# Optimization experiments

Hardware: AMD Instinct MI355X
Metric: run time of the kernel (lower is better)

The kernel has to match this reference:

```python
import jax, jax.numpy as jnp
import numpy as np

# Standard SMPL kinematic tree (parent of each of the 24 joints)
PARENTS = np.array([-1, 0, 0, 0, 1, 2, 3, 4, 5, 6, 7, 8, 9, 9, 9, 12, 13, 14, 16, 17, 18, 19, 20, 21])
B, V, NJ = 512, 6890, 24


def rodrigues(r):
    # r: (N,3) axis-angle -> (N,3,3) rotation matrices
    theta = jnp.linalg.norm(r, axis=1, keepdims=True) + 1e-8  # (N,1), eps mirrors the noise trick in torch code
    rh = r / theta                                            # (N,3) unit axis
    x, y, z = rh[:, 0], rh[:, 1], rh[:, 2]
    zero = jnp.zeros_like(x)
    K = jnp.stack([zero, -z, y, z, zero, -x, -y, x, zero], axis=1).reshape(-1, 3, 3)
    cos = jnp.cos(theta)[:, :, None]
    sin = jnp.sin(theta)[:, :, None]
    outer = rh[:, :, None] * rh[:, None, :]
    I3 = jnp.eye(3, dtype=r.dtype)
    return cos * I3 + (1.0 - cos) * outer + sin * K


def _make_A(Ri, ti):
    # Ri: (B,3,3), ti: (B,3) -> homogeneous (B,4,4)
    Rt = jnp.concatenate([Ri, ti[:, :, None]], axis=2)  # (B,3,4)
    bottom = jnp.broadcast_to(jnp.array([0.0, 0.0, 0.0, 1.0], dtype=Ri.dtype), (Ri.shape[0], 1, 4))
    return jnp.concatenate([Rt, bottom], axis=1)


def smpl_forward(betas, pose, trans, v_template, shapedirs, posedirs, J_regressor, joint_regressor, weights):
    b = betas.shape[0]
    # shape blend shapes
    v_shaped = jnp.einsum('bs,vcs->bvc', betas, shapedirs) + v_template  # (B,V,3)
    J = jnp.einsum('jv,bvc->bjc', J_regressor, v_shaped)                 # (B,24,3)
    R = rodrigues(pose.reshape(-1, 3)).reshape(b, NJ, 3, 3)              # (B,24,3,3)
    I3 = jnp.eye(3, dtype=pose.dtype)
    lrotmin = (R[:, 1:] - I3).reshape(b, (NJ - 1) * 9)                   # (B,207)
    v_posed = v_shaped + jnp.einsum('bp,vcp->bvc', lrotmin, posedirs)    # pose blend shapes
    # forward kinematics along the chain (fixed 24-joint loop)
    Gs = [_make_A(R[:, 0], J[:, 0])]
    for i in range(1, NJ):
        p = int(PARENTS[i])
        Gs.append(jnp.matmul(Gs[p], _make_A(R[:, i], J[:, i] - J[:, p])))
    G = jnp.stack(Gs, axis=1)                                            # (B,24,4,4)
    # remove rest-pose joint locations (the 'pack' subtraction)
    Jh = jnp.concatenate([J, jnp.zeros((b, NJ, 1), dtype=J.dtype)], axis=2)  # (B,24,4)
    t = jnp.einsum('bjxy,bjy->bjx', G, Jh)                               # (B,24,4)
    G = G - jnp.pad(t[..., None], ((0, 0), (0, 0), (0, 0), (3, 0)))      # subtract in last column
    # linear blend skinning
    T = jnp.einsum('bjxy,vj->bvxy', G, weights)                          # (B,V,4,4) -- large, memory bound
    vh = jnp.concatenate([v_posed, jnp.ones((b, v_posed.shape[1], 1), dtype=v_posed.dtype)], axis=2)
    v = jnp.einsum('bvxy,bvy->bvx', T, vh)[..., :3]                      # (B,V,3)
    result = v + trans[:, None, :]
    joints = jnp.einsum('bvc,jv->bjc', result, joint_regressor)          # (B,24,3)
    return result, joints


def setup_inputs() -> dict:
    key = jax.random.key(0)
    ks = jax.random.split(key, 9)
    betas = jax.random.normal(ks[0], (B, 10), dtype=jnp.float32)
    pose = jax.random.normal(ks[1], (B, 72), dtype=jnp.float32) * 0.3
    trans = jax.random.normal(ks[2], (B, 3), dtype=jnp.float32)
    v_template = jax.random.normal(ks[3], (V, 3), dtype=jnp.float32) * 0.3
    shapedirs = jax.random.normal(ks[4], (V, 3, 10), dtype=jnp.float32) * 0.01
    posedirs = jax.random.normal(ks[5], (V, 3, 207), dtype=jnp.float32) * 0.01
    Jr = jax.random.uniform(ks[6], (NJ, V), dtype=jnp.float32)
    J_regressor = Jr / jnp.sum(Jr, axis=1, keepdims=True)
    jr2 = jax.random.uniform(ks[7], (NJ, V), dtype=jnp.float32)
    joint_regressor = jr2 / jnp.sum(jr2, axis=1, keepdims=True)
    w = jax.random.uniform(ks[8], (V, NJ), dtype=jnp.float32)
    weights = w / jnp.sum(w, axis=1, keepdims=True)
    return {"betas": betas, "pose": pose, "trans": trans, "v_template": v_template,
            "shapedirs": shapedirs, "posedirs": posedirs, "J_regressor": J_regressor,
            "joint_regressor": joint_regressor, "weights": weights}


def reference(betas, pose, trans, v_template, shapedirs, posedirs, J_regressor, joint_regressor, weights):
    return smpl_forward(betas, pose, trans, v_template, shapedirs, posedirs, J_regressor, joint_regressor, weights)
```

## Files before the change

kernel.cpp:

```cpp
#include <hip/hip_runtime.h>
#include <hip/hip_bf16.h>

#define VNUM 6890
#define VPAD 6912
#define BNUM 512
#define NJ 24

typedef short bf16x8 __attribute__((ext_vector_type(8)));
typedef float f32x4 __attribute__((ext_vector_type(4)));

__device__ __forceinline__ short f2bf(float x) {
    union { float f; unsigned u; } v; v.f = x;
    unsigned r = v.u + 0x7fff + ((v.u >> 16) & 1);
    return (short)(r >> 16);
}

#define WS_JS 0
#define WS_LWX 800
#define WS_GA 58144
#define WS_WT 156448
#define WS_PB 267040
#define WS_PART 267040

#define RES_ELEMS (512 * 6890 * 3)

__global__ __launch_bounds__(256) void ka_kernel(const float* __restrict__ Jr,
                                                 const float* __restrict__ sd,
                                                 const float* __restrict__ vt,
                                                 float* __restrict__ part) {
    int j = blockIdx.x;
    int ch = blockIdx.y;
    int tid = threadIdx.x;
    int vbeg = ch * 864;
    int vend = min(vbeg + 864, VNUM);
    float acc[33];
#pragma unroll
    for (int k = 0; k < 33; ++k) acc[k] = 0.f;
    for (int v = vbeg + tid; v < vend; v += 256) {
        float q = Jr[j * VNUM + v];
#pragma unroll
        for (int c = 0; c < 3; ++c) {
#pragma unroll
            for (int s = 0; s < 10; ++s)
                acc[c * 11 + s] += q * sd[v * 30 + c * 10 + s];
            acc[c * 11 + 10] += q * vt[v * 3 + c];
        }
    }
#pragma unroll
    for (int k = 0; k < 33; ++k) {
        float a = acc[k];
#pragma unroll
        for (int off = 32; off >= 1; off >>= 1) a += __shfl_xor(a, off);
        acc[k] = a;
    }
    __shared__ float red[4][33];
    int lane = tid & 63, wid = tid >> 6;
    if (lane == 0) {
#pragma unroll
        for (int k = 0; k < 33; ++k) red[wid][k] = acc[k];
    }
    __syncthreads();
    if (tid < 33)
        part[(j * 8 + ch) * 33 + tid] = red[0][tid] + red[1][tid] + red[2][tid] + red[3][tid];
}

__global__ __launch_bounds__(64) void ka2_kernel(const float* __restrict__ part,
                                                 float* __restrict__ js) {
    int j = blockIdx.x;
    int t = threadIdx.x;
    if (t < 33) {
        float a = 0.f;
#pragma unroll
        for (int ch = 0; ch < 8; ++ch) a += part[(j * 8 + ch) * 33 + t];
        js[j * 33 + t] = a;
    }
}

__global__ __launch_bounds__(64) void kb_kernel(const float* __restrict__ pose,
                                                const float* __restrict__ betas,
                                                const float* __restrict__ trans,
                                                const float* __restrict__ js,
                                                short* __restrict__ lwX,
                                                short* __restrict__ ga) {
    int b = blockIdx.x;
    int t = threadIdx.x;
    __shared__ float Rl[24][9];
    __shared__ float Jl[24][3];
    __shared__ float Gl[24][12];

    if (t < 24) {
        float x = pose[b * 72 + t * 3 + 0];
        float y = pose[b * 72 + t * 3 + 1];
        float z = pose[b * 72 + t * 3 + 2];
        float th = sqrtf(x * x + y * y + z * z) + 1e-8f;
        float rx = x / th, ry = y / th, rz = z / th;
        float cs = cosf(th), sn = sinf(th), mc = 1.f - cs;
        float R[9];
        R[0] = cs + mc * rx * rx;      R[1] = mc * rx * ry - sn * rz; R[2] = mc * rx * rz + sn * ry;
        R[3] = mc * ry * rx + sn * rz; R[4] = cs + mc * ry * ry;      R[5] = mc * ry * rz - sn * rx;
        R[6] = mc * rz * rx - sn * ry; R[7] = mc * rz * ry + sn * rx; R[8] = cs + mc * rz * rz;
#pragma unroll
        for (int k = 0; k < 9; ++k) Rl[t][k] = R[k];
        if (t >= 1) {
#pragma unroll
            for (int k = 0; k < 9; ++k)
                lwX[b * 224 + (t - 1) * 9 + k] =
                    f2bf(R[k] - ((k == 0 || k == 4 || k == 8) ? 1.f : 0.f));
        }
#pragma unroll
        for (int c = 0; c < 3; ++c) {
            float a = js[(t * 3 + c) * 11 + 10];
#pragma unroll
            for (int s = 0; s < 10; ++s) a += betas[b * 10 + s] * js[(t * 3 + c) * 11 + s];
            Jl[t][c] = a;
        }
    } else if (t >= 32 && t < 42) {
        lwX[b * 224 + 207 + (t - 32)] = f2bf(betas[b * 10 + (t - 32)]);
    } else if (t == 42) {
        lwX[b * 224 + 217] = f2bf(1.f);
    } else if (t >= 43 && t < 49) {
        lwX[b * 224 + 218 + (t - 43)] = 0;
    }
    __syncthreads();

    if (t < 12) {
        int x = t >> 2, yy = t & 3;
        Gl[0][t] = (yy < 3) ? Rl[0][x * 3 + yy] : Jl[0][x];
    }
    __syncthreads();

    const int par[24] = {-1, 0, 0, 0, 1, 2, 3, 4, 5, 6, 7, 8, 9, 9, 9, 12, 13, 14, 16, 17, 18, 19, 20, 21};
#pragma unroll
    for (int i = 1; i < 24; ++i) {
        if (t < 12) {
            int x = t >> 2, yy = t & 3;
            int p = par[i];
            float a0, a1, a2, add;
            if (yy < 3) {
                a0 = Rl[i][0 * 3 + yy]; a1 = Rl[i][1 * 3 + yy]; a2 = Rl[i][2 * 3 + yy]; add = 0.f;
            } else {
                a0 = Jl[i][0] - Jl[p][0]; a1 = Jl[i][1] - Jl[p][1]; a2 = Jl[i][2] - Jl[p][2];
                add = Gl[p][x * 4 + 3];
            }
            Gl[i][t] = Gl[p][x * 4 + 0] * a0 + Gl[p][x * 4 + 1] * a1 + Gl[p][x * 4 + 2] * a2 + add;
        }
        __syncthreads();
    }

    if (t < 24) {
#pragma unroll
        for (int x = 0; x < 3; ++x) {
            float tx = Gl[t][x * 4 + 0] * Jl[t][0] + Gl[t][x * 4 + 1] * Jl[t][1] + Gl[t][x * 4 + 2] * Jl[t][2];
#pragma unroll
            for (int yy = 0; yy < 3; ++yy)
                ga[(x * 4 + yy) * (512 * 32) + b * 32 + t] = f2bf(Gl[t][x * 4 + yy]);
            ga[(x * 4 + 3) * (512 * 32) + b * 32 + t] =
                f2bf(Gl[t][x * 4 + 3] - tx + trans[b * 3 + x]);
        }
    } else if (t < 32) {
#pragma unroll
        for (int r = 0; r < 12; ++r) ga[r * (512 * 32) + b * 32 + t] = 0;
    }
}

__global__ __launch_bounds__(256) void pe_kernel(const float* __restrict__ pd,
                                                 const float* __restrict__ sd,
                                                 const float* __restrict__ vt,
                                                 short* __restrict__ pb) {
    int v0 = blockIdx.x * 32;
    int c = blockIdx.y;
    int t = threadIdx.x;
    int vloc = t >> 3, sub = t & 7;
    int v = v0 + vloc;
    short* dst = pb + ((size_t)c * VPAD + v) * 224;
    if (v < VNUM) {
        const float* pr = pd + (size_t)v * 621 + c * 207;
        const float* sr = sd + (size_t)v * 30 + c * 10;
        float vtv = vt[v * 3 + c];
#pragma unroll
        for (int i = 0; i < 28; ++i) {
            int k = sub + i * 8;
            float val;
            if (k < 207) val = pr[k];
            else if (k < 217) val = sr[k - 207];
            else if (k == 217) val = vtv;
            else val = 0.f;
            dst[k] = f2bf(val);
        }
    } else {
#pragma unroll
        for (int i = 0; i < 28; ++i) dst[sub + i * 8] = 0;
    }
}

__global__ __launch_bounds__(256) void wp_kernel(const float* __restrict__ w,
                                                 short* __restrict__ wt) {
    int v = blockIdx.x * 256 + threadIdx.x;
    if (v >= VPAD) return;
    short* dst = wt + (size_t)v * 32;
    if (v < VNUM) {
#pragma unroll
        for (int j = 0; j < 24; ++j) dst[j] = f2bf(w[(size_t)v * 24 + j]);
#pragma unroll
        for (int j = 24; j < 32; ++j) dst[j] = 0;
    } else {
#pragma unroll
        for (int j = 0; j < 32; ++j) dst[j] = 0;
    }
}

__global__ __launch_bounds__(256) void km_kernel(const short* __restrict__ lwX,
                                                 const short* __restrict__ pb,
                                                 const short* __restrict__ ga,
                                                 const short* __restrict__ wt,
                                                 float* __restrict__ out) {
    int tid = threadIdx.x;
    int lane = tid & 63;
    int wid = tid >> 6;
    int row = lane & 15;
    int kq = lane >> 4;
    int b0 = blockIdx.x * 32;
    int v0 = blockIdx.y * 128 + wid * 32;

    f32x4 vp[2][2][3];
#pragma unroll
    for (int m = 0; m < 2; ++m)
#pragma unroll
        for (int vb = 0; vb < 2; ++vb)
#pragma unroll
            for (int c = 0; c < 3; ++c) vp[m][vb][c] = (f32x4){0.f, 0.f, 0.f, 0.f};

    const short* arow0 = lwX + (b0 + row) * 224 + kq * 8;
    const short* arow1 = arow0 + 16 * 224;
#pragma unroll
    for (int ks = 0; ks < 7; ++ks) {
        bf16x8 a0 = *(const bf16x8*)(arow0 + ks * 32);
        bf16x8 a1 = *(const bf16x8*)(arow1 + ks * 32);
#pragma unroll
        for (int vb = 0; vb < 2; ++vb) {
#pragma unroll
            for (int c = 0; c < 3; ++c) {
                bf16x8 bf = *(const bf16x8*)(pb + ((size_t)c * VPAD + v0 + vb * 16 + row) * 224 +
                                             ks * 32 + kq * 8);
                vp[0][vb][c] = __builtin_amdgcn_mfma_f32_16x16x32_bf16(a0, bf, vp[0][vb][c], 0, 0, 0);
                vp[1][vb][c] = __builtin_amdgcn_mfma_f32_16x16x32_bf16(a1, bf, vp[1][vb][c], 0, 0, 0);
            }
        }
    }

    bf16x8 wfrag[2];
#pragma unroll
    for (int vb = 0; vb < 2; ++vb)
        wfrag[vb] = *(const bf16x8*)(wt + (size_t)(v0 + vb * 16 + row) * 32 + kq * 8);

    const f32x4 zero4 = {0.f, 0.f, 0.f, 0.f};
    int brow = kq * 4;

    float resAll[2][2][4][3];

#pragma unroll
    for (int x = 0; x < 3; ++x) {
        f32x4 res[2][2];
        {
            int r = x * 4 + 3;
            bf16x8 g0 = *(const bf16x8*)(ga + ((size_t)r * 512 + b0 + row) * 32 + kq * 8);
            bf16x8 g1 = *(const bf16x8*)(ga + ((size_t)r * 512 + b0 + 16 + row) * 32 + kq * 8);
#pragma unroll
            for (int vb = 0; vb < 2; ++vb) {
                res[0][vb] = __builtin_amdgcn_mfma_f32_16x16x32_bf16(g0, wfrag[vb], zero4, 0, 0, 0);
                res[1][vb] = __builtin_amdgcn_mfma_f32_16x16x32_bf16(g1, wfrag[vb], zero4, 0, 0, 0);
            }
        }
#pragma unroll
        for (int y = 0; y < 3; ++y) {
            int r = x * 4 + y;
            bf16x8 g0 = *(const bf16x8*)(ga + ((size_t)r * 512 + b0 + row) * 32 + kq * 8);
            bf16x8 g1 = *(const bf16x8*)(ga + ((size_t)r * 512 + b0 + 16 + row) * 32 + kq * 8);
#pragma unroll
            for (int vb = 0; vb < 2; ++vb) {
                f32x4 t0 = __builtin_amdgcn_mfma_f32_16x16x32_bf16(g0, wfrag[vb], zero4, 0, 0, 0);
                f32x4 t1 = __builtin_amdgcn_mfma_f32_16x16x32_bf16(g1, wfrag[vb], zero4, 0, 0, 0);
#pragma unroll
                for (int reg = 0; reg < 4; ++reg) {
                    res[0][vb][reg] += t0[reg] * vp[0][vb][y][reg];
                    res[1][vb][reg] += t1[reg] * vp[1][vb][y][reg];
                }
            }
        }
#pragma unroll
        for (int m = 0; m < 2; ++m)
#pragma unroll
            for (int vb = 0; vb < 2; ++vb)
#pragma unroll
                for (int reg = 0; reg < 4; ++reg)
                    resAll[m][vb][reg][x] = res[m][vb][reg];
    }

#pragma unroll
    for (int m = 0; m < 2; ++m) {
#pragma unroll
        for (int vb = 0; vb < 2; ++vb) {
            int v = v0 + vb * 16 + row;
            if (v < VNUM) {
#pragma unroll
                for (int reg = 0; reg < 4; ++reg) {
                    int b = b0 + m * 16 + brow + reg;
                    float* op = out + ((size_t)b * VNUM + v) * 3;
                    op[0] = resAll[m][vb][reg][0];
                    op[1] = resAll[m][vb][reg][1];
                    op[2] = resAll[m][vb][reg][2];
                }
            }
        }
    }
}

__global__ __launch_bounds__(256) void kd_kernel(const float* __restrict__ res,
                                                 const float* __restrict__ jr2,
                                                 float* __restrict__ joints) {
    int b = blockIdx.x;
    int tid = threadIdx.x;
    float acc[24][3];
#pragma unroll
    for (int j = 0; j < 24; ++j)
#pragma unroll
        for (int c = 0; c < 3; ++c) acc[j][c] = 0.f;

    const float* rb = res + (size_t)b * VNUM * 3;
    for (int v = tid; v < VNUM; v += 256) {
        float r0 = rb[v * 3 + 0];
        float r1 = rb[v * 3 + 1];
        float r2 = rb[v * 3 + 2];
#pragma unroll
        for (int j = 0; j < 24; ++j) {
            float q = jr2[(size_t)j * VNUM + v];
            acc[j][0] += q * r0;
            acc[j][1] += q * r1;
            acc[j][2] += q * r2;
        }
    }
#pragma unroll
    for (int j = 0; j < 24; ++j)
#pragma unroll
        for (int c = 0; c < 3; ++c) {
            float a = acc[j][c];
#pragma unroll
            for (int off = 32; off >= 1; off >>= 1) a += __shfl_xor(a, off);
            acc[j][c] = a;
        }
    __shared__ float red[4][72];
    int lane = tid & 63, wid = tid >> 6;
    if (lane == 0) {
#pragma unroll
        for (int j = 0; j < 24; ++j)
#pragma unroll
            for (int c = 0; c < 3; ++c) red[wid][j * 3 + c] = acc[j][c];
    }
    __syncthreads();
    if (tid < 72)
        joints[(size_t)b * 72 + tid] = red[0][tid] + red[1][tid] + red[2][tid] + red[3][tid];
}

extern "C" void kernel_launch(void* const* d_in, const int* in_sizes, int n_in,
                              void* d_out, int out_size, void* d_ws, size_t ws_size,
                              hipStream_t stream) {
    const float* betas = (const float*)d_in[0];
    const float* pose = (const float*)d_in[1];
    const float* trans = (const float*)d_in[2];
    const float* v_template = (const float*)d_in[3];
    const float* shapedirs = (const float*)d_in[4];
    const float* posedirs = (const float*)d_in[5];
    const float* J_regressor = (const float*)d_in[6];
    const float* joint_regressor = (const float*)d_in[7];
    const float* weights = (const float*)d_in[8];
    float* out = (float*)d_out;

    float* wsf = (float*)d_ws;
    float* js = wsf + WS_JS;
    float* part = wsf + WS_PART;
    short* lwX = (short*)(wsf + WS_LWX);
    short* ga = (short*)(wsf + WS_GA);
    short* wt = (short*)(wsf + WS_WT);
    short* pb = (short*)(wsf + WS_PB);

    ka_kernel<<<dim3(24, 8), 256, 0, stream>>>(J_regressor, shapedirs, v_template, part);
    ka2_kernel<<<24, 64, 0, stream>>>(part, js);
    pe_kernel<<<dim3(216, 3), 256, 0, stream>>>(posedirs, shapedirs, v_template, pb);
    wp_kernel<<<27, 256, 0, stream>>>(weights, wt);
    kb_kernel<<<512, 64, 0, stream>>>(pose, betas, trans, js, lwX, ga);
    km_kernel<<<dim3(16, 54), 256, 0, stream>>>(lwX, pb, ga, wt, out);
    kd_kernel<<<512, 256, 0, stream>>>(out, joint_regressor, out + RES_ELEMS);
}
```

Before: 106.8 us.

## Remap km blocks across XCDs and split joint regression over joints with atomics

The main km kernel now runs on a 1D grid whose block index is remapped so that vertex-tile rows are grouped per XCD (block index mod 8). This is meant to improve L2 locality for the shared posedirs and weights tiles. The kd joint-regression kernel is restructured so each block handles two batches, one quarter of the vertices, and six joints per wave, with partial sums combined by atomicAdd into an output zeroed by a new memset. This raises parallelism and reuses each regressor load across two batches, at the cost of extra atomics, a memset, and nondeterministic summation order.

```diff
diff --git a/kernel.cpp b/kernel.cpp
--- a/kernel.cpp
+++ b/kernel.cpp
@@ -214,13 +214,20 @@
                                                  const short* __restrict__ ga,
                                                  const short* __restrict__ wt,
                                                  float* __restrict__ out) {
+    int d = blockIdx.x;
+    int xcd = d & 7;
+    int q = d >> 3;
+    int by = (q >> 4) * 8 + xcd;
+    int bx = q & 15;
+    if (by >= 54) return;
+
     int tid = threadIdx.x;
     int lane = tid & 63;
     int wid = tid >> 6;
     int row = lane & 15;
     int kq = lane >> 4;
-    int b0 = blockIdx.x * 32;
-    int v0 = blockIdx.y * 128 + wid * 32;
+    int b0 = bx * 32;
+    int v0 = by * 128 + wid * 32;
 
     f32x4 vp[2][2][3];
 #pragma unroll
@@ -318,47 +325,55 @@
 __global__ __launch_bounds__(256) void kd_kernel(const float* __restrict__ res,
                                                  const float* __restrict__ jr2,
                                                  float* __restrict__ joints) {
-    int b = blockIdx.x;
+    int bp = blockIdx.x;
+    int q = blockIdx.y;
     int tid = threadIdx.x;
-    float acc[24][3];
-#pragma unroll
-    for (int j = 0; j < 24; ++j)
-#pragma unroll
-        for (int c = 0; c < 3; ++c) acc[j][c] = 0.f;
-
-    const float* rb = res + (size_t)b * VNUM * 3;
-    for (int v = tid; v < VNUM; v += 256) {
-        float r0 = rb[v * 3 + 0];
-        float r1 = rb[v * 3 + 1];
-        float r2 = rb[v * 3 + 2];
-#pragma unroll
-        for (int j = 0; j < 24; ++j) {
-            float q = jr2[(size_t)j * VNUM + v];
-            acc[j][0] += q * r0;
-            acc[j][1] += q * r1;
-            acc[j][2] += q * r2;
-        }
-    }
-#pragma unroll
-    for (int j = 0; j < 24; ++j)
-#pragma unroll
-        for (int c = 0; c < 3; ++c) {
-            float a = acc[j][c];
-#pragma unroll
-            for (int off = 32; off >= 1; off >>= 1) a += __shfl_xor(a, off);
-            acc[j][c] = a;
-        }
-    __shared__ float red[4][72];
-    int lane = tid & 63, wid = tid >> 6;
-    if (lane == 0) {
-#pragma unroll
-        for (int j = 0; j < 24; ++j)
-#pragma unroll
-            for (int c = 0; c < 3; ++c) red[wid][j * 3 + c] = acc[j][c];
-    }
-    __syncthreads();
-    if (tid < 72)
-        joints[(size_t)b * 72 + tid] = red[0][tid] + red[1][tid] + red[2][tid] + red[3][tid];
+    int lane = tid & 63;
+    int w = tid >> 6;
+    int b0 = bp * 2;
+    int j0 = w * 6;
+
+    float acc[2][6][3];
+#pragma unroll
+    for (int bb = 0; bb < 2; ++bb)
+#pragma unroll
+        for (int jj = 0; jj < 6; ++jj)
+#pragma unroll
+            for (int c = 0; c < 3; ++c) acc[bb][jj][c] = 0.f;
+
+    const float* rb0 = res + (size_t)b0 * VNUM * 3;
+    const float* rb1 = rb0 + (size_t)VNUM * 3;
+    int vbase = q * 1728 + lane;
+    for (int i = 0; i < 27; ++i) {
+        int v = vbase + i * 64;
+        if (v < VNUM) {
+            float r00 = rb0[v * 3 + 0], r01 = rb0[v * 3 + 1], r02 = rb0[v * 3 + 2];
+            float r10 = rb1[v * 3 + 0], r11 = rb1[v * 3 + 1], r12 = rb1[v * 3 + 2];
+#pragma unroll
+            for (int jj = 0; jj < 6; ++jj) {
+                float qv = jr2[(size_t)(j0 + jj) * VNUM + v];
+                acc[0][jj][0] += qv * r00;
+                acc[0][jj][1] += qv * r01;
+                acc[0][jj][2] += qv * r02;
+                acc[1][jj][0] += qv * r10;
+                acc[1][jj][1] += qv * r11;
+                acc[1][jj][2] += qv * r12;
+            }
+        }
+    }
+
+#pragma unroll
+    for (int bb = 0; bb < 2; ++bb)
+#pragma unroll
+        for (int jj = 0; jj < 6; ++jj)
+#pragma unroll
+            for (int c = 0; c < 3; ++c) {
+                float a = acc[bb][jj][c];
+#pragma unroll
+                for (int off = 32; off >= 1; off >>= 1) a += __shfl_xor(a, off);
+                if (lane == 0)
+                    atomicAdd(&joints[(size_t)(b0 + bb) * 72 + (j0 + jj) * 3 + c], a);
+            }
 }
 
 extern "C" void kernel_launch(void* const* d_in, const int* in_sizes, int n_in,
@@ -383,11 +398,13 @@
     short* wt = (short*)(wsf + WS_WT);
     short* pb = (short*)(wsf + WS_PB);
 
+    hipMemsetAsync((void*)(out + RES_ELEMS), 0, (size_t)512 * 72 * 4, stream);
+
     ka_kernel<<<dim3(24, 8), 256, 0, stream>>>(J_regressor, shapedirs, v_template, part);
     ka2_kernel<<<24, 64, 0, stream>>>(part, js);
     pe_kernel<<<dim3(216, 3), 256, 0, stream>>>(posedirs, shapedirs, v_template, pb);
     wp_kernel<<<27, 256, 0, stream>>>(weights, wt);
     kb_kernel<<<512, 64, 0, stream>>>(pose, betas, trans, js, lwX, ga);
-    km_kernel<<<dim3(16, 54), 256, 0, stream>>>(lwX, pb, ga, wt, out);
-    kd_kernel<<<512, 256, 0, stream>>>(out, joint_regressor, out + RES_ELEMS);
-}
+    km_kernel<<<896, 256, 0, stream>>>(lwX, pb, ga, wt, out);
+    kd_kernel<<<dim3(256, 4), 256, 0, stream>>>(out, joint_regressor, out + RES_ELEMS);
+}
```

Result: no change. 108.7 us (+1.8%).
